# Kernel tuning notes

Hardware: AMD Instinct MI355X
Metric: run time of the kernel (lower is better)

## Reference

```python
import jax, jax.numpy as jnp
import numpy as np

NUM_FIELDS = 26
VOCAB = 100000
B = 16384
D = 64            # embedding_dim
BM1, BM2 = 128, 64    # bottom_mlp_sizes
TM1, TM2 = 256, 1     # top mlp hidden/out (top_mlp_sizes=[512,256,1] -> Linear(415,256),ReLU,Linear(256,1))
NUM_FEATS = NUM_FIELDS + 1
NUM_INTER = NUM_FEATS * (NUM_FEATS - 1) // 2   # 351
TOP_IN = NUM_INTER + BM2                        # 415


def setup_inputs() -> dict:
    key = jax.random.key(0)
    ks = jax.random.split(key, 13)
    x_cat = jax.random.randint(ks[0], (NUM_FIELDS, B), 0, VOCAB)
    price = jax.random.normal(ks[1], (B,), dtype=jnp.float32)
    emb_tables = jax.random.normal(ks[2], (NUM_FIELDS, VOCAB, D), dtype=jnp.float32) * 0.05
    Wp = jax.random.normal(ks[3], (1, D), dtype=jnp.float32) * 0.1
    bp = jnp.zeros((D,), jnp.float32)
    W1 = jax.random.normal(ks[4], (D, BM1), dtype=jnp.float32) * 0.1
    b1 = jnp.zeros((BM1,), jnp.float32)
    W2 = jax.random.normal(ks[5], (BM1, BM2), dtype=jnp.float32) * 0.1
    b2 = jnp.zeros((BM2,), jnp.float32)
    Wt1 = jax.random.normal(ks[6], (TOP_IN, TM1), dtype=jnp.float32) * 0.05
    bt1 = jnp.zeros((TM1,), jnp.float32)
    Wt2 = jax.random.normal(ks[7], (TM1, TM2), dtype=jnp.float32) * 0.05
    bt2 = jnp.zeros((TM2,), jnp.float32)
    return {"x_cat": x_cat, "price": price, "emb_tables": emb_tables,
            "Wp": Wp, "bp": bp, "W1": W1, "b1": b1, "W2": W2, "b2": b2,
            "Wt1": Wt1, "bt1": bt1, "Wt2": Wt2, "bt2": bt2}


# precomputed upper-triangular (i<j, row-major) index pairs -- matches the torch double loop order
_IU, _JU = np.triu_indices(NUM_FEATS, k=1)


def reference(x_cat, price, emb_tables, Wp, bp, W1, b1, W2, b2, Wt1, bt1, Wt2, bt2):
    # embedding gathers: [F, B, D] -> [B, F, D]
    emb = emb_tables[jnp.arange(NUM_FIELDS)[:, None], x_cat]
    emb = jnp.transpose(emb, (1, 0, 2))
    # dense (price) projection: [B, D]
    dense_embed = price[:, None] @ Wp + bp
    # all features: [B, F+1, D]
    feats = jnp.concatenate([emb, dense_embed[:, None, :]], axis=1)
    # pairwise dot products via batched Gram matrix, then triangular gather
    gram = jnp.einsum('bid,bjd->bij', feats, feats)          # [B, 27, 27]
    interactions = gram[:, _IU, _JU]                          # [B, 351]
    # bottom MLP on dense embedding
    h = jax.nn.relu(dense_embed @ W1 + b1)
    dense_out = jax.nn.relu(h @ W2 + b2)                      # [B, 64]
    # top MLP
    concat = jnp.concatenate([interactions, dense_out], axis=1)  # [B, 415]
    t = jax.nn.relu(concat @ Wt1 + bt1)
    out = (t @ Wt2 + bt2)[:, 0]                               # [B]
    return out
```

## Files before the change

kernel.cpp:

```cpp
#include <hip/hip_runtime.h>
#include <hip/hip_bf16.h>
#include <cstdint>

#define NUM_FIELDS 26
#define VOCAB      100000
#define BATCH      16384
#define CK         416
#define CS_STRIDE  424

typedef __attribute__((ext_vector_type(8)))  short bf16x8_t;
typedef __attribute__((ext_vector_type(16))) float f32x16_t;

__device__ __forceinline__ short f2bf(float x) {
  unsigned u = __builtin_bit_cast(unsigned, x);
  u += 0x7FFFu + ((u >> 16) & 1u);
  return (short)(u >> 16);
}

__global__ __launch_bounds__(128) void k0_prep(
    const float* __restrict__ Wp, const float* __restrict__ bp,
    const float* __restrict__ W1, const float* __restrict__ b1,
    const float* __restrict__ W2, const float* __restrict__ b2,
    const float* __restrict__ Wt1,
    float* __restrict__ bps, float* __restrict__ PQ, short* __restrict__ wt1t) {
  if (blockIdx.x != 0) {
    const int n = blockIdx.x - 1;
    for (int k = threadIdx.x; k < CK; k += 128) {
      float v = (k < 415) ? Wt1[(size_t)k * 256 + n] : 0.f;
      wt1t[(size_t)n * CK + k] = f2bf(v);
    }
    return;
  }
  __shared__ float u1s[128], c1s[128], ts[128];
  __shared__ int ord[128];
  const int j = threadIdx.x;
  float u = 0.f, c = 0.f;
  for (int d = 0; d < 64; ++d) {
    float w = W1[d * 128 + j];
    u = fmaf(Wp[d], w, u);
    c = fmaf(bp[d], w, c);
  }
  c += b1[j];
  u1s[j] = u; c1s[j] = c;
  ts[j] = (u != 0.f) ? (-c / u) : __builtin_inff();
  __syncthreads();
  const float tj = ts[j];
  int r = 0;
  for (int i = 0; i < 128; ++i) {
    float ti = ts[i];
    if (ti < tj || (ti == tj && i < j)) ++r;
  }
  ord[r] = j;
  __syncthreads();
  bps[j] = ts[ord[j]];
  if (j < 64) {
    const int d = j;
    float P = 0.f, Q = b2[d];
    for (int k = 0; k < 128; ++k) {
      float uk = u1s[k];
      bool act = (uk < 0.f) || (uk == 0.f && c1s[k] > 0.f);
      if (act) {
        float w = W2[k * 64 + d];
        P = fmaf(uk, w, P);
        Q = fmaf(c1s[k], w, Q);
      }
    }
    PQ[d] = P; PQ[129 * 64 + d] = Q;
    for (int seg = 1; seg <= 128; ++seg) {
      int jk = ord[seg - 1];
      float uk = u1s[jk], ck = c1s[jk];
      float sgn = (uk > 0.f) ? 1.f : ((uk < 0.f) ? -1.f : 0.f);
      float w = W2[jk * 64 + d] * sgn;
      P = fmaf(uk, w, P);
      Q = fmaf(ck, w, Q);
      PQ[seg * 64 + d] = P;
      PQ[129 * 64 + seg * 64 + d] = Q;
    }
  }
}

__global__ __launch_bounds__(512, 4) void k1_fused(
    const int* __restrict__ x_cat, const float* __restrict__ price,
    const float* __restrict__ emb, const float* __restrict__ Wp,
    const float* __restrict__ bp_, const float* __restrict__ bps_g,
    const float* __restrict__ PQ, const short* __restrict__ wt1t,
    const float* __restrict__ bt1, const float* __restrict__ Wt2,
    const float* __restrict__ bt2, float* __restrict__ out) {
  __shared__ __align__(16) short Fb[8][32 * 72];
  __shared__ __align__(16) short Cs[32][CS_STRIDE];
  __shared__ float partial_s[8][32];
  __shared__ float bps_s[128];
  const int tid = threadIdx.x, lane = tid & 63, w = tid >> 6;
  if (tid < 128) bps_s[tid] = bps_g[tid];
  {
    int* zp = (int*)&Fb[w][27 * 72];
    for (int i = lane; i < 180; i += 64) zp[i] = 0;
  }
  __syncthreads();
  const float wpv = Wp[lane], bpv = bp_[lane];
  const int r16 = lane >> 4, c4 = (lane & 15) * 4;
  const int row = lane & 31, kh = lane >> 5;
  const int koff = kh * 8;
  for (int it = 0; it < 4; ++it) {
    const int sm = w * 4 + it;
    const int s = blockIdx.x * 32 + sm;
    const float pr = price[s];
    int idxv = 0;
    if (lane < NUM_FIELDS) idxv = x_cat[lane * BATCH + s];
    #pragma unroll
    for (int g = 0; g < 6; ++g) {
      const int r = g * 4 + r16;
      const int idx = __shfl(idxv, r, 64);
      const float4 v = *(const float4*)&emb[((size_t)r * VOCAB + idx) * 64 + c4];
      union { short s4[4]; uint2 u; } t;
      t.s4[0] = f2bf(v.x); t.s4[1] = f2bf(v.y); t.s4[2] = f2bf(v.z); t.s4[3] = f2bf(v.w);
      *(uint2*)&Fb[w][r * 72 + c4] = t.u;
    }
    {
      const int r = 24 + (r16 & 1);
      const int idx = __shfl(idxv, r, 64);
      if (lane < 32) {
        const float4 v = *(const float4*)&emb[((size_t)r * VOCAB + idx) * 64 + c4];
        union { short s4[4]; uint2 u; } t;
        t.s4[0] = f2bf(v.x); t.s4[1] = f2bf(v.y); t.s4[2] = f2bf(v.z); t.s4[3] = f2bf(v.w);
        *(uint2*)&Fb[w][r * 72 + c4] = t.u;
      }
    }
    Fb[w][26 * 72 + lane] = f2bf(fmaf(pr, wpv, bpv));
    bf16x8_t a0 = *(const bf16x8_t*)&Fb[w][row * 72 +  0 + koff];
    bf16x8_t a1 = *(const bf16x8_t*)&Fb[w][row * 72 + 16 + koff];
    bf16x8_t a2 = *(const bf16x8_t*)&Fb[w][row * 72 + 32 + koff];
    bf16x8_t a3 = *(const bf16x8_t*)&Fb[w][row * 72 + 48 + koff];
    f32x16_t acc = {0.f,0.f,0.f,0.f,0.f,0.f,0.f,0.f,0.f,0.f,0.f,0.f,0.f,0.f,0.f,0.f};
    acc = __builtin_amdgcn_mfma_f32_32x32x16_bf16(a0, a0, acc, 0, 0, 0);
    acc = __builtin_amdgcn_mfma_f32_32x32x16_bf16(a1, a1, acc, 0, 0, 0);
    acc = __builtin_amdgcn_mfma_f32_32x32x16_bf16(a2, a2, acc, 0, 0, 0);
    acc = __builtin_amdgcn_mfma_f32_32x32x16_bf16(a3, a3, acc, 0, 0, 0);
    int lo = 0, hi = 128;
    while (lo < hi) { int mid = (lo + hi) >> 1; if (bps_s[mid] < pr) lo = mid + 1; else hi = mid; }
    float dv = fmaf(pr, PQ[lo * 64 + lane], PQ[129 * 64 + lo * 64 + lane]);
    dv = fmaxf(dv, 0.f);
    Cs[sm][351 + lane] = f2bf(dv);
    if (lane == 0) Cs[sm][415] = 0;
    const int jc = row, rh = kh * 4;
    #pragma unroll
    for (int reg = 0; reg < 16; ++reg) {
      int i = (reg & 3) + 8 * (reg >> 2) + rh;
      if (i < jc && jc < 27) {
        int p = 26 * i - (i * (i - 1)) / 2 + (jc - i - 1);
        Cs[sm][p] = f2bf(acc[reg]);
      }
    }
  }
  __syncthreads();
  const int n0 = w * 32;
  const short* bp0 = wt1t + (size_t)(n0 + row) * CK + koff;
  f32x16_t tacc = {0.f,0.f,0.f,0.f,0.f,0.f,0.f,0.f,0.f,0.f,0.f,0.f,0.f,0.f,0.f,0.f};
  #pragma unroll
  for (int k0 = 0; k0 < CK; k0 += 16) {
    bf16x8_t a = *(const bf16x8_t*)&Cs[row][k0 + koff];
    bf16x8_t b = *(const bf16x8_t*)(bp0 + k0);
    tacc = __builtin_amdgcn_mfma_f32_32x32x16_bf16(a, b, tacc, 0, 0, 0);
  }
  const int n = n0 + row;
  const float bt1v = bt1[n], w2v = Wt2[n];
  float ps[16];
  #pragma unroll
  for (int r = 0; r < 16; ++r) ps[r] = fmaxf(tacc[r] + bt1v, 0.f) * w2v;
  #pragma unroll
  for (int d = 1; d <= 16; d <<= 1) {
    #pragma unroll
    for (int r = 0; r < 16; ++r) ps[r] += __shfl_xor(ps[r], d, 64);
  }
  if (row == 0) {
    #pragma unroll
    for (int r = 0; r < 16; ++r)
      partial_s[w][(r & 3) + 8 * (r >> 2) + 4 * kh] = ps[r];
  }
  __syncthreads();
  if (tid < 32) {
    float ssum = bt2[0];
    #pragma unroll
    for (int ww = 0; ww < 8; ++ww) ssum += partial_s[ww][tid];
    out[blockIdx.x * 32 + tid] = ssum;
  }
}

extern "C" void kernel_launch(void* const* d_in, const int* in_sizes, int n_in,
                              void* d_out, int out_size, void* d_ws, size_t ws_size,
                              hipStream_t stream) {
  const int*   x_cat = (const int*)d_in[0];
  const float* price = (const float*)d_in[1];
  const float* emb   = (const float*)d_in[2];
  const float* Wp    = (const float*)d_in[3];
  const float* bp    = (const float*)d_in[4];
  const float* W1    = (const float*)d_in[5];
  const float* b1    = (const float*)d_in[6];
  const float* W2    = (const float*)d_in[7];
  const float* b2    = (const float*)d_in[8];
  const float* Wt1   = (const float*)d_in[9];
  const float* bt1   = (const float*)d_in[10];
  const float* Wt2   = (const float*)d_in[11];
  const float* bt2   = (const float*)d_in[12];
  float* out = (float*)d_out;

  float* ws   = (float*)d_ws;
  float* PQ   = ws;
  float* bps  = ws + 16512;
  short* wt1t = (short*)(ws + 16640);

  k0_prep <<<dim3(257), dim3(128), 0, stream>>>(Wp, bp, W1, b1, W2, b2, Wt1, bps, PQ, wt1t);
  k1_fused<<<dim3(BATCH / 32), dim3(512), 0, stream>>>(x_cat, price, emb, Wp, bp,
                                                       bps, PQ, wt1t, bt1, Wt2, bt2, out);
}
```

Baseline: 814.8 us.

## Gather embeddings directly into MFMA registers with double-buffered prefetch

Each lane now loads its own embedding row slice straight into registers in the MFMA operand layout, which removes the per-wave LDS staging buffer and its round trip. The next sample's gather is prefetched while the current one is computed, overlapping global latency with the Gram MFMAs. The breakpoint binary search over LDS is replaced by two ballot/popcount comparisons, and the dense embedding is precomputed into a small LDS tile. The cost is higher register pressure from holding 16 float4 prefetch registers per lane, which may reduce occupancy.

```diff
diff --git a/kernel.cpp b/kernel.cpp
--- a/kernel.cpp
+++ b/kernel.cpp
@@ -86,58 +86,78 @@
     const float* __restrict__ PQ, const short* __restrict__ wt1t,
     const float* __restrict__ bt1, const float* __restrict__ Wt2,
     const float* __restrict__ bt2, float* __restrict__ out) {
-  __shared__ __align__(16) short Fb[8][32 * 72];
   __shared__ __align__(16) short Cs[32][CS_STRIDE];
+  __shared__ __align__(16) short Db[32][64];
   __shared__ float partial_s[8][32];
-  __shared__ float bps_s[128];
   const int tid = threadIdx.x, lane = tid & 63, w = tid >> 6;
-  if (tid < 128) bps_s[tid] = bps_g[tid];
-  {
-    int* zp = (int*)&Fb[w][27 * 72];
-    for (int i = lane; i < 180; i += 64) zp[i] = 0;
-  }
-  __syncthreads();
-  const float wpv = Wp[lane], bpv = bp_[lane];
-  const int r16 = lane >> 4, c4 = (lane & 15) * 4;
+  const int s0 = blockIdx.x * 32;
+
+  for (int i = tid; i < 2048; i += 512) {
+    int sm = i >> 6, d = i & 63;
+    Db[sm][d] = f2bf(fmaf(price[s0 + sm], Wp[d], bp_[d]));
+  }
+
   const int row = lane & 31, kh = lane >> 5;
   const int koff = kh * 8;
+  const float blo = bps_g[lane], bhi = bps_g[64 + lane];
+
+  const int sb = s0 + w * 4;
+  const bool gat = (row < NUM_FIELDS);
+  int4 idx4 = make_int4(0, 0, 0, 0);
+  if (gat) idx4 = *(const int4*)&x_cat[(size_t)row * BATCH + sb];
+  const float4 pr4 = *(const float4*)&price[sb];
+  const int   idxs[4] = {idx4.x, idx4.y, idx4.z, idx4.w};
+  const float prs[4]  = {pr4.x, pr4.y, pr4.z, pr4.w};
+
+  __syncthreads();
+
+  float4 vv[2][8];
+  if (gat) {
+    const float* rb = emb + ((size_t)row * VOCAB + idxs[0]) * 64 + koff;
+    #pragma unroll
+    for (int q = 0; q < 4; ++q) {
+      vv[0][2 * q]     = *(const float4*)(rb + 16 * q);
+      vv[0][2 * q + 1] = *(const float4*)(rb + 16 * q + 4);
+    }
+  }
+  #pragma unroll
   for (int it = 0; it < 4; ++it) {
+    const int cur = it & 1, nxt = cur ^ 1;
+    if (it < 3 && gat) {
+      const float* rb = emb + ((size_t)row * VOCAB + idxs[it + 1]) * 64 + koff;
+      #pragma unroll
+      for (int q = 0; q < 4; ++q) {
+        vv[nxt][2 * q]     = *(const float4*)(rb + 16 * q);
+        vv[nxt][2 * q + 1] = *(const float4*)(rb + 16 * q + 4);
+      }
+    }
     const int sm = w * 4 + it;
-    const int s = blockIdx.x * 32 + sm;
-    const float pr = price[s];
-    int idxv = 0;
-    if (lane < NUM_FIELDS) idxv = x_cat[lane * BATCH + s];
-    #pragma unroll
-    for (int g = 0; g < 6; ++g) {
-      const int r = g * 4 + r16;
-      const int idx = __shfl(idxv, r, 64);
-      const float4 v = *(const float4*)&emb[((size_t)r * VOCAB + idx) * 64 + c4];
-      union { short s4[4]; uint2 u; } t;
-      t.s4[0] = f2bf(v.x); t.s4[1] = f2bf(v.y); t.s4[2] = f2bf(v.z); t.s4[3] = f2bf(v.w);
-      *(uint2*)&Fb[w][r * 72 + c4] = t.u;
-    }
-    {
-      const int r = 24 + (r16 & 1);
-      const int idx = __shfl(idxv, r, 64);
-      if (lane < 32) {
-        const float4 v = *(const float4*)&emb[((size_t)r * VOCAB + idx) * 64 + c4];
-        union { short s4[4]; uint2 u; } t;
-        t.s4[0] = f2bf(v.x); t.s4[1] = f2bf(v.y); t.s4[2] = f2bf(v.z); t.s4[3] = f2bf(v.w);
-        *(uint2*)&Fb[w][r * 72 + c4] = t.u;
-      }
-    }
-    Fb[w][26 * 72 + lane] = f2bf(fmaf(pr, wpv, bpv));
-    bf16x8_t a0 = *(const bf16x8_t*)&Fb[w][row * 72 +  0 + koff];
-    bf16x8_t a1 = *(const bf16x8_t*)&Fb[w][row * 72 + 16 + koff];
-    bf16x8_t a2 = *(const bf16x8_t*)&Fb[w][row * 72 + 32 + koff];
-    bf16x8_t a3 = *(const bf16x8_t*)&Fb[w][row * 72 + 48 + koff];
+    bf16x8_t a[4];
+    if (gat) {
+      #pragma unroll
+      for (int q = 0; q < 4; ++q) {
+        const float4 x = vv[cur][2 * q], y = vv[cur][2 * q + 1];
+        bf16x8_t t;
+        t[0] = f2bf(x.x); t[1] = f2bf(x.y); t[2] = f2bf(x.z); t[3] = f2bf(x.w);
+        t[4] = f2bf(y.x); t[5] = f2bf(y.y); t[6] = f2bf(y.z); t[7] = f2bf(y.w);
+        a[q] = t;
+      }
+    } else if (row == 26) {
+      #pragma unroll
+      for (int q = 0; q < 4; ++q)
+        a[q] = *(const bf16x8_t*)&Db[sm][16 * q + koff];
+    } else {
+      #pragma unroll
+      for (int q = 0; q < 4; ++q)
+        a[q] = (bf16x8_t){0, 0, 0, 0, 0, 0, 0, 0};
+    }
     f32x16_t acc = {0.f,0.f,0.f,0.f,0.f,0.f,0.f,0.f,0.f,0.f,0.f,0.f,0.f,0.f,0.f,0.f};
-    acc = __builtin_amdgcn_mfma_f32_32x32x16_bf16(a0, a0, acc, 0, 0, 0);
-    acc = __builtin_amdgcn_mfma_f32_32x32x16_bf16(a1, a1, acc, 0, 0, 0);
-    acc = __builtin_amdgcn_mfma_f32_32x32x16_bf16(a2, a2, acc, 0, 0, 0);
-    acc = __builtin_amdgcn_mfma_f32_32x32x16_bf16(a3, a3, acc, 0, 0, 0);
-    int lo = 0, hi = 128;
-    while (lo < hi) { int mid = (lo + hi) >> 1; if (bps_s[mid] < pr) lo = mid + 1; else hi = mid; }
+    acc = __builtin_amdgcn_mfma_f32_32x32x16_bf16(a[0], a[0], acc, 0, 0, 0);
+    acc = __builtin_amdgcn_mfma_f32_32x32x16_bf16(a[1], a[1], acc, 0, 0, 0);
+    acc = __builtin_amdgcn_mfma_f32_32x32x16_bf16(a[2], a[2], acc, 0, 0, 0);
+    acc = __builtin_amdgcn_mfma_f32_32x32x16_bf16(a[3], a[3], acc, 0, 0, 0);
+    const float pr = prs[it];
+    const int lo = __popcll(__ballot(blo < pr)) + __popcll(__ballot(bhi < pr));
     float dv = fmaf(pr, PQ[lo * 64 + lane], PQ[129 * 64 + lo * 64 + lane]);
     dv = fmaxf(dv, 0.f);
     Cs[sm][351 + lane] = f2bf(dv);
@@ -158,9 +178,9 @@
   f32x16_t tacc = {0.f,0.f,0.f,0.f,0.f,0.f,0.f,0.f,0.f,0.f,0.f,0.f,0.f,0.f,0.f,0.f};
   #pragma unroll
   for (int k0 = 0; k0 < CK; k0 += 16) {
-    bf16x8_t a = *(const bf16x8_t*)&Cs[row][k0 + koff];
-    bf16x8_t b = *(const bf16x8_t*)(bp0 + k0);
-    tacc = __builtin_amdgcn_mfma_f32_32x32x16_bf16(a, b, tacc, 0, 0, 0);
+    bf16x8_t aa = *(const bf16x8_t*)&Cs[row][k0 + koff];
+    bf16x8_t bb = *(const bf16x8_t*)(bp0 + k0);
+    tacc = __builtin_amdgcn_mfma_f32_32x32x16_bf16(aa, bb, tacc, 0, 0, 0);
   }
   const int n = n0 + row;
   const float bt1v = bt1[n], w2v = Wt2[n];
```

Result: no change. 822.2 us (+0.9%).
